# Kernel tuning notes

Measured on AMD Instinct MI355X. Metric: run time of the kernel, lower is better.

The kernel has to match this reference:

```python
import jax, jax.numpy as jnp
import numpy as np

N_NODES = 100000


def spmm(edge_src, edge_dst, edge_w, h):
    # out[d] = sum_{e: dst[e]=d} w[e] * h[src[e]]  -- sparse adj @ h
    return jax.ops.segment_sum(h[edge_src] * edge_w[:, None], edge_dst,
                               num_segments=N_NODES)


def gcn_layer(x, W, edge_src, edge_dst, edge_w, use_activation):
    support = x @ W                      # dense projection [N, out]
    out = spmm(edge_src, edge_dst, edge_w, support)
    return jax.nn.relu(out) if use_activation else out


def setup_inputs() -> dict:
    key = jax.random.key(0)
    ks = jax.random.split(key, 9)
    n_edges = 3200000

    def xavier(k, shape):
        fan_in, fan_out = shape
        a = jnp.sqrt(6.0 / (fan_in + fan_out))
        return jax.random.uniform(k, shape, jnp.float32, -a, a)

    return {
        "x": jax.random.normal(ks[0], (N_NODES, 512), jnp.float32),
        "edge_src": jax.random.randint(ks[1], (n_edges,), 0, N_NODES, jnp.int32),
        "edge_dst": jax.random.randint(ks[2], (n_edges,), 0, N_NODES, jnp.int32),
        "edge_w": jax.random.uniform(ks[3], (n_edges,), jnp.float32),
        "W1": xavier(ks[4], (512, 128)),
        "W2": xavier(ks[5], (128, 64)),
        "W3": xavier(ks[6], (64, 32)),
        "Wmu": xavier(ks[7], (32, 16)),
        "Wlv": xavier(ks[8], (32, 16)),
    }


def reference(x, edge_src, edge_dst, edge_w, W1, W2, W3, Wmu, Wlv):
    # Eval-mode GCNVAE forward: dropout is identity, z = mu.
    h1 = gcn_layer(x, W1, edge_src, edge_dst, edge_w, True)
    h2 = gcn_layer(h1, W2, edge_src, edge_dst, edge_w, True)
    h3 = gcn_layer(h2, W3, edge_src, edge_dst, edge_w, True)
    mu = gcn_layer(h3, Wmu, edge_src, edge_dst, edge_w, False)
    logvar = gcn_layer(h3, Wlv, edge_src, edge_dst, edge_w, False)
    z = mu  # reparameterize in eval mode returns mu
    return (z, mu, logvar)
```

## Files before the change

### kernel.cpp

```cpp
#include <hip/hip_runtime.h>

typedef __attribute__((ext_vector_type(4))) float floatx4;
typedef __attribute__((ext_vector_type(8))) short bf16x8;

#define NPB 256
#define CHUNK 6144
#define MAXB 12288

__device__ __forceinline__ float bf2f(unsigned short h) {
  union { unsigned int u; float f; } c; c.u = ((unsigned int)h) << 16; return c.f;
}
__device__ __forceinline__ unsigned short f2bf(float f) {
  union { float f; unsigned int u; } c; c.f = f;
  unsigned int r = c.u + 0x7FFFu + ((c.u >> 16) & 1u);
  return (unsigned short)(r >> 16);
}

__device__ __forceinline__ void gl16(const void* g, void* l) {
  __builtin_amdgcn_global_load_lds(
      (const __attribute__((address_space(1))) unsigned int*)g,
      (__attribute__((address_space(3))) unsigned int*)l, 16, 0, 0);
}


__global__ __launch_bounds__(256) void bhist_k(const int* __restrict__ dst,
                                               int* __restrict__ bcnt, int E, int B) {
  __shared__ int h[512];
  int tid = threadIdx.x;
  for (int i = tid; i < 512; i += 256) h[i] = 0;
  __syncthreads();
  for (int i = blockIdx.x * 256 + tid; i < E; i += gridDim.x * 256)
    atomicAdd(&h[dst[i] >> 8], 1);
  __syncthreads();
  for (int i = tid; i < B; i += 256)
    if (h[i]) atomicAdd(&bcnt[i], h[i]);
}

__global__ __launch_bounds__(512) void bscan_k(const int* __restrict__ bcnt,
                                               int* __restrict__ bstart,
                                               int* __restrict__ bcur, int B) {
  __shared__ int s[512];
  int tid = threadIdx.x;
  int v = (tid < B) ? bcnt[tid] : 0;
  s[tid] = v;
  __syncthreads();
  for (int off = 1; off < 512; off <<= 1) {
    int t = (tid >= off) ? s[tid - off] : 0;
    __syncthreads();
    s[tid] += t;
    __syncthreads();
  }
  int excl = s[tid] - v;
  if (tid < B) { bstart[tid] = excl; bcur[tid] = excl; }
  if (tid == 511) bstart[B] = s[511];
}

__global__ __launch_bounds__(256) void part_k(const int* __restrict__ src,
                                              const int* __restrict__ dst,
                                              const float* __restrict__ w,
                                              int* __restrict__ bcur,
                                              int2* __restrict__ prec, int E, int B) {
  __shared__ int hist[512];
  __shared__ int lstart[512];
  __shared__ int cur[512];
  __shared__ int gbase[512];
  __shared__ int ss[256];
  __shared__ int2 srt[CHUNK];
  int tid = threadIdx.x;
  int e0 = blockIdx.x * CHUNK;
  int cnt = min(CHUNK, E - e0);
  for (int i = tid; i < 512; i += 256) hist[i] = 0;
  __syncthreads();
  for (int i = tid; i < cnt; i += 256) atomicAdd(&hist[dst[e0 + i] >> 8], 1);
  __syncthreads();
  int a0 = hist[2 * tid], a1 = hist[2 * tid + 1];
  ss[tid] = a0 + a1;
  __syncthreads();
  for (int off = 1; off < 256; off <<= 1) {
    int t = (tid >= off) ? ss[tid - off] : 0;
    __syncthreads();
    ss[tid] += t;
    __syncthreads();
  }
  int excl = tid ? ss[tid - 1] : 0;
  lstart[2 * tid] = excl;     cur[2 * tid] = excl;
  lstart[2 * tid + 1] = excl + a0; cur[2 * tid + 1] = excl + a0;
  __syncthreads();
  for (int i = tid; i < B; i += 256)
    gbase[i] = hist[i] ? atomicAdd(&bcur[i], hist[i]) : 0;
  __syncthreads();
  for (int i = tid; i < cnt; i += 256) {
    int d = dst[e0 + i];
    int b = d >> 8;
    float wf = w[e0 + i];
    int w15 = (int)(wf * 32768.f + 0.5f);
    if (w15 > 32767) w15 = 32767;
    int2 r;
    r.x = src[e0 + i] | (w15 << 17);
    r.y = (b << 8) | (d & 255);
    int pos = atomicAdd(&cur[b], 1);
    srt[pos] = r;
  }
  __syncthreads();
  for (int j = tid; j < cnt; j += 256) {
    int2 r = srt[j];
    int b = r.y >> 8;
    prec[gbase[b] + (j - lstart[b])] = make_int2(r.x, r.y & 255);
  }
}

__global__ __launch_bounds__(256) void sort_k(const int2* __restrict__ prec,
                                              const int* __restrict__ bstart,
                                              unsigned int* __restrict__ recs,
                                              int* __restrict__ row_start,
                                              int* __restrict__ counts, int N, int B) {
  __shared__ int hist[256], lstart[256], cur[256], ss[256];
  __shared__ unsigned int srt[MAXB];
  int b = blockIdx.x;
  int tid = threadIdx.x;
  int s = bstart[b];
  int cnt = bstart[b + 1] - s;
  if (cnt > MAXB) cnt = MAXB;
  hist[tid] = 0;
  __syncthreads();
  for (int i = tid; i < cnt; i += 256) atomicAdd(&hist[prec[s + i].y], 1);
  __syncthreads();
  ss[tid] = hist[tid];
  __syncthreads();
  for (int off = 1; off < 256; off <<= 1) {
    int t = (tid >= off) ? ss[tid - off] : 0;
    __syncthreads();
    ss[tid] += t;
    __syncthreads();
  }
  int excl = ss[tid] - hist[tid];
  lstart[tid] = excl;
  cur[tid] = excl;
  int node = b * NPB + tid;
  if (node < N) { row_start[node] = s + excl; counts[node] = hist[tid]; }
  __syncthreads();
  for (int i = tid; i < cnt; i += 256) {
    int2 r = prec[s + i];
    int pos = atomicAdd(&cur[r.y], 1);
    srt[pos] = (unsigned int)r.x;
  }
  __syncthreads();
  for (int i = tid; i < cnt; i += 256) recs[s + i] = srt[i];
}


__global__ __launch_bounds__(256) void tw1_k(const float* __restrict__ W1,
                                             unsigned short* __restrict__ W1t) {
  int i = blockIdx.x * 256 + threadIdx.x;
  if (i >= 512 * 128) return;
  int k = i >> 7, n = i & 127;
  W1t[n * 512 + k] = f2bf(W1[i]);
}


__device__ __forceinline__ bf16x8 cvt8(float4 lo, float4 hi) {
  bf16x8 r;
  r[0] = (short)f2bf(lo.x); r[1] = (short)f2bf(lo.y);
  r[2] = (short)f2bf(lo.z); r[3] = (short)f2bf(lo.w);
  r[4] = (short)f2bf(hi.x); r[5] = (short)f2bf(hi.y);
  r[6] = (short)f2bf(hi.z); r[7] = (short)f2bf(hi.w);
  return r;
}

__global__ __launch_bounds__(256, 3) void gemm1_mfma(const float* __restrict__ A,
                                                     const unsigned short* __restrict__ W1t,
                                                     unsigned short* __restrict__ C, int N) {
  constexpr int BK = 32;
  __shared__ __align__(16) float          As[2][128 * BK];
  __shared__ __align__(16) unsigned short Bs[2][128 * BK];
  int tid = threadIdx.x;
  int lane = tid & 63;
  int w = tid >> 6;
  int m0 = lane & 15;
  int kq = lane >> 4;
  int rowBase = blockIdx.x * 128;

  floatx4 acc[8][2];
#pragma unroll
  for (int i = 0; i < 8; ++i)
#pragma unroll
    for (int j = 0; j < 2; ++j) acc[i][j] = (floatx4)0.f;

  size_t aSrc[4]; int aDst[4];
#pragma unroll
  for (int it = 0; it < 4; ++it) {
    int c = it * 256 + w * 64 + lane;
    int r = c >> 3, ch = c & 7;
    int sc = ch ^ (r & 7);
    int gr = rowBase + r;
    if (gr > N - 1) gr = N - 1;
    aSrc[it] = (size_t)gr * 512 + sc * 4;
    aDst[it] = (it * 256 + w * 64) * 4;
  }
  size_t bSrc[2]; int bDst[2];
#pragma unroll
  for (int it = 0; it < 2; ++it) {
    int c = it * 256 + w * 64 + lane;
    int n = c >> 2, ch = c & 3;
    bSrc[it] = (size_t)n * 512 + ch * 8;
    bDst[it] = (it * 256 + w * 64) * 8;
  }

  auto stage = [&](int bi, int k0) {
#pragma unroll
    for (int it = 0; it < 4; ++it) gl16(&A[aSrc[it] + k0], &As[bi][aDst[it]]);
#pragma unroll
    for (int it = 0; it < 2; ++it) gl16(&W1t[bSrc[it] + k0], &Bs[bi][bDst[it]]);
  };

  stage(0, 0);
  int cur = 0;
  for (int t = 0; t < 16; ++t) {
    if (t < 15) {
      stage(cur ^ 1, (t + 1) * BK);
      asm volatile("s_waitcnt vmcnt(6)" ::: "memory");
    } else {
      asm volatile("s_waitcnt vmcnt(0)" ::: "memory");
    }
    __builtin_amdgcn_s_barrier();

    bf16x8 bb0 = *reinterpret_cast<const bf16x8*>(&Bs[cur][(w * 32 + m0) * BK + kq * 8]);
    bf16x8 bb1 = *reinterpret_cast<const bf16x8*>(&Bs[cur][(w * 32 + 16 + m0) * BK + kq * 8]);
#pragma unroll
    for (int mi = 0; mi < 8; ++mi) {
      int row = mi * 16 + m0;
      int s = row & 7;
      float4 lo = *reinterpret_cast<const float4*>(&As[cur][row * BK + (((2 * kq) ^ s) << 2)]);
      float4 hi = *reinterpret_cast<const float4*>(&As[cur][row * BK + (((2 * kq + 1) ^ s) << 2)]);
      bf16x8 a = cvt8(lo, hi);
      acc[mi][0] = __builtin_amdgcn_mfma_f32_16x16x32_bf16(a, bb0, acc[mi][0], 0, 0, 0);
      acc[mi][1] = __builtin_amdgcn_mfma_f32_16x16x32_bf16(a, bb1, acc[mi][1], 0, 0, 0);
    }
    __builtin_amdgcn_s_barrier();
    cur ^= 1;
  }

#pragma unroll
  for (int mi = 0; mi < 8; ++mi) {
#pragma unroll
    for (int jn = 0; jn < 2; ++jn) {
      int gc = w * 32 + jn * 16 + m0;
#pragma unroll
      for (int p = 0; p < 4; ++p) {
        int gr = rowBase + mi * 16 + kq * 4 + p;
        if (gr < N) C[(size_t)gr * 128 + gc] = f2bf(acc[mi][jn][p]);
      }
    }
  }
}


template <int K, int O>
__global__ __launch_bounds__(256) void gemm_kernel(const unsigned short* __restrict__ A,
                                                   const float* __restrict__ W,
                                                   unsigned short* __restrict__ C, int N) {
  constexpr int BM = 64;
  constexpr int BK = 32;
  constexpr int TM = 4;
  constexpr int TN = O / 16;
  __shared__ float As[BK][BM];
  __shared__ float Ws[BK][O];
  int tid = threadIdx.x;
  int tx = tid % 16;
  int ty = tid / 16;
  int rowBase = blockIdx.x * BM;
  float acc[TM][TN];
#pragma unroll
  for (int i = 0; i < TM; ++i)
#pragma unroll
    for (int j = 0; j < TN; ++j) acc[i][j] = 0.f;

  for (int k0 = 0; k0 < K; k0 += BK) {
    {
      int r = tid >> 2;
      int kc = (tid & 3) * 8;
      int gr = rowBase + r;
      uint4 v = make_uint4(0u, 0u, 0u, 0u);
      if (gr < N) v = *reinterpret_cast<const uint4*>(&A[(size_t)gr * K + k0 + kc]);
      const unsigned short* pv = reinterpret_cast<const unsigned short*>(&v);
#pragma unroll
      for (int j = 0; j < 8; ++j) As[kc + j][r] = bf2f(pv[j]);
    }
    {
      constexpr int ELEMS = BK * O / 256;
      constexpr int NV = ELEMS / 4;
#pragma unroll
      for (int it = 0; it < NV; ++it) {
        int linear = (tid + it * 256) * 4;
        int kk = linear / O;
        int oo = linear % O;
        float4 v = *reinterpret_cast<const float4*>(&W[(size_t)(k0 + kk) * O + oo]);
        Ws[kk][oo + 0] = v.x; Ws[kk][oo + 1] = v.y;
        Ws[kk][oo + 2] = v.z; Ws[kk][oo + 3] = v.w;
      }
    }
    __syncthreads();
#pragma unroll
    for (int k = 0; k < BK; ++k) {
      float a[TM], w[TN];
#pragma unroll
      for (int i = 0; i < TM; ++i) a[i] = As[k][ty * TM + i];
#pragma unroll
      for (int j = 0; j < TN; ++j) w[j] = Ws[k][tx * TN + j];
#pragma unroll
      for (int i = 0; i < TM; ++i)
#pragma unroll
        for (int j = 0; j < TN; ++j) acc[i][j] += a[i] * w[j];
    }
    __syncthreads();
  }
#pragma unroll
  for (int i = 0; i < TM; ++i) {
    int gr = rowBase + ty * TM + i;
    if (gr >= N) continue;
#pragma unroll
    for (int j = 0; j < TN; j += 2) {
      unsigned int p = ((unsigned int)f2bf(acc[i][j + 1]) << 16) | f2bf(acc[i][j]);
      *reinterpret_cast<unsigned int*>(&C[(size_t)gr * O + tx * TN + j]) = p;
    }
  }
}


#define INV32768 3.0517578125e-05f

template <int O, bool RELU>
__global__ __launch_bounds__(256) void spmm_kernel(const unsigned int* __restrict__ recs,
                                                   const int* __restrict__ row_start,
                                                   const int* __restrict__ counts,
                                                   const unsigned short* __restrict__ sup,
                                                   unsigned short* __restrict__ hout, int N) {
  constexpr int SUBW = O / 2;
  constexpr int NPW = 256 / SUBW;
  constexpr int U = 8;
  int tid = threadIdx.x;
  int lane = tid % SUBW;
  int sub = tid / SUBW;
  int node = blockIdx.x * NPW + sub;
  if (node >= N) return;
  int start = row_start[node];
  int deg = counts[node];
  const unsigned int* supu = reinterpret_cast<const unsigned int*>(sup);
  const unsigned int* rp = recs + start;
  float a0 = 0.f, a1 = 0.f;
  int i = 0;
  for (; i + U <= deg; i += U) {
    unsigned int r[U];
#pragma unroll
    for (int j = 0; j < U; ++j) r[j] = rp[i + j];
    unsigned int v[U];
#pragma unroll
    for (int j = 0; j < U; ++j) v[j] = supu[(size_t)(r[j] & 0x1FFFFu) * (O / 2) + lane];
#pragma unroll
    for (int j = 0; j < U; ++j) {
      float w = (float)(r[j] >> 17) * INV32768;
      a0 += w * bf2f((unsigned short)(v[j] & 0xFFFFu));
      a1 += w * bf2f((unsigned short)(v[j] >> 16));
    }
  }
  for (; i < deg; ++i) {
    unsigned int rec = rp[i];
    float w = (float)(rec >> 17) * INV32768;
    unsigned int v = supu[(size_t)(rec & 0x1FFFFu) * (O / 2) + lane];
    a0 += w * bf2f((unsigned short)(v & 0xFFFFu));
    a1 += w * bf2f((unsigned short)(v >> 16));
  }
  if (RELU) { a0 = fmaxf(a0, 0.f); a1 = fmaxf(a1, 0.f); }
  unsigned int p = ((unsigned int)f2bf(a1) << 16) | f2bf(a0);
  reinterpret_cast<unsigned int*>(hout)[(size_t)node * (O / 2) + lane] = p;
}

__global__ __launch_bounds__(256) void spmm_mulv_kernel(const unsigned int* __restrict__ recs,
                                                        const int* __restrict__ row_start,
                                                        const int* __restrict__ counts,
                                                        const unsigned short* __restrict__ sup,
                                                        float* __restrict__ out, int N) {
  constexpr int SUBW = 16;
  constexpr int NPW = 256 / SUBW;
  constexpr int U = 8;
  int tid = threadIdx.x;
  int lane = tid % SUBW;
  int sub = tid / SUBW;
  int node = blockIdx.x * NPW + sub;
  if (node >= N) return;
  int start = row_start[node];
  int deg = counts[node];
  const unsigned int* supu = reinterpret_cast<const unsigned int*>(sup);
  const unsigned int* rp = recs + start;
  float a0 = 0.f, a1 = 0.f;
  int i = 0;
  for (; i + U <= deg; i += U) {
    unsigned int r[U];
#pragma unroll
    for (int j = 0; j < U; ++j) r[j] = rp[i + j];
    unsigned int v[U];
#pragma unroll
    for (int j = 0; j < U; ++j) v[j] = supu[(size_t)(r[j] & 0x1FFFFu) * 16 + lane];
#pragma unroll
    for (int j = 0; j < U; ++j) {
      float w = (float)(r[j] >> 17) * INV32768;
      a0 += w * bf2f((unsigned short)(v[j] & 0xFFFFu));
      a1 += w * bf2f((unsigned short)(v[j] >> 16));
    }
  }
  for (; i < deg; ++i) {
    unsigned int rec = rp[i];
    float w = (float)(rec >> 17) * INV32768;
    unsigned int v = supu[(size_t)(rec & 0x1FFFFu) * 16 + lane];
    a0 += w * bf2f((unsigned short)(v & 0xFFFFu));
    a1 += w * bf2f((unsigned short)(v >> 16));
  }
  size_t nf = (size_t)N * 16;
  if (lane < 8) {
    float2 p = make_float2(a0, a1);
    *reinterpret_cast<float2*>(&out[(size_t)node * 16 + lane * 2]) = p;
    *reinterpret_cast<float2*>(&out[nf + (size_t)node * 16 + lane * 2]) = p;
  } else {
    int l = lane - 8;
    *reinterpret_cast<float2*>(&out[2 * nf + (size_t)node * 16 + l * 2]) =
        make_float2(a0, a1);
  }
}

__global__ void packw_k(const float* __restrict__ Wmu,
                        const float* __restrict__ Wlv,
                        float* __restrict__ Wcat) {
  int i = blockIdx.x * 256 + threadIdx.x;
  if (i >= 32 * 32) return;
  int k = i / 32, o = i % 32;
  Wcat[i] = (o < 16) ? Wmu[k * 16 + o] : Wlv[k * 16 + (o - 16)];
}


extern "C" void kernel_launch(void* const* d_in, const int* in_sizes, int n_in,
                              void* d_out, int out_size, void* d_ws, size_t ws_size,
                              hipStream_t stream) {
  const float* x    = (const float*)d_in[0];
  const int* esrc   = (const int*)d_in[1];
  const int* edst   = (const int*)d_in[2];
  const float* ew   = (const float*)d_in[3];
  const float* W1   = (const float*)d_in[4];
  const float* W2   = (const float*)d_in[5];
  const float* W3   = (const float*)d_in[6];
  const float* Wmu  = (const float*)d_in[7];
  const float* Wlv  = (const float*)d_in[8];
  float* out = (float*)d_out;
  int N = in_sizes[0] / 512;
  int E = in_sizes[1];
  int B = (N + NPB - 1) / NPB;

  char* p = (char*)d_ws;
  auto alloc = [&](size_t bytes) -> char* {
    char* r = p;
    p += (bytes + 255) & ~(size_t)255;
    return r;
  };
  int*  counts = (int*)alloc((size_t)N * 4);
  int*  rowst  = (int*)alloc((size_t)N * 4);
  int*  bcnt   = (int*)alloc((size_t)(B + 1) * 4);
  int*  bstart = (int*)alloc((size_t)(B + 1) * 4);
  int*  bcur   = (int*)alloc((size_t)(B + 1) * 4);
  int2* prec   = (int2*)alloc((size_t)E * 8);
  unsigned int* recs = (unsigned int*)alloc((size_t)E * 4);
  unsigned short* bufA = (unsigned short*)alloc((size_t)N * 128 * 2);
  unsigned short* bufB = (unsigned short*)alloc((size_t)N * 128 * 2);
  unsigned short* W1t  = (unsigned short*)alloc(512 * 128 * 2);
  float* Wcat = (float*)alloc(32 * 32 * 4);

  hipMemsetAsync(bcnt, 0, (size_t)(B + 1) * 4, stream);
  bhist_k<<<256, 256, 0, stream>>>(edst, bcnt, E, B);
  bscan_k<<<1, 512, 0, stream>>>(bcnt, bstart, bcur, B);
  part_k<<<(E + CHUNK - 1) / CHUNK, 256, 0, stream>>>(esrc, edst, ew, bcur, prec, E, B);
  sort_k<<<B, 256, 0, stream>>>(prec, bstart, recs, rowst, counts, N, B);

  tw1_k<<<256, 256, 0, stream>>>(W1, W1t);
  gemm1_mfma<<<(N + 127) / 128, 256, 0, stream>>>(x, W1t, bufA, N);
  spmm_kernel<128, true><<<(N + 3) / 4, 256, 0, stream>>>(recs, rowst, counts, bufA, bufB, N);

  int gemmGrid = (N + 63) / 64;

  gemm_kernel<128, 64><<<gemmGrid, 256, 0, stream>>>(bufB, W2, bufA, N);
  spmm_kernel<64, true><<<(N + 7) / 8, 256, 0, stream>>>(recs, rowst, counts, bufA, bufB, N);

  gemm_kernel<64, 32><<<gemmGrid, 256, 0, stream>>>(bufB, W3, bufA, N);
  spmm_kernel<32, true><<<(N + 15) / 16, 256, 0, stream>>>(recs, rowst, counts, bufA, bufB, N);

  packw_k<<<4, 256, 0, stream>>>(Wmu, Wlv, Wcat);
  gemm_kernel<32, 32><<<gemmGrid, 256, 0, stream>>>(bufB, Wcat, bufA, N);
  spmm_mulv_kernel<<<(N + 15) / 16, 256, 0, stream>>>(recs, rowst, counts, bufA, out, N);
}
```

Baseline: 770.2 us.

## Rework SpMM to one wavefront per node, shrink sort buckets, enlarge GEMM tiles

```diff
diff --git a/kernel.cpp b/kernel.cpp
--- a/kernel.cpp
+++ b/kernel.cpp
@@ -3,9 +3,10 @@
 typedef __attribute__((ext_vector_type(4))) float floatx4;
 typedef __attribute__((ext_vector_type(8))) short bf16x8;
 
-#define NPB 256
-#define CHUNK 6144
-#define MAXB 12288
+#define NPB 128
+#define NBINS 1024
+#define CHUNK 4096
+#define MAXB 6144
 
 __device__ __forceinline__ float bf2f(unsigned short h) {
   union { unsigned int u; float f; } c; c.u = ((unsigned int)h) << 16; return c.f;
@@ -25,26 +26,26 @@
 
 __global__ __launch_bounds__(256) void bhist_k(const int* __restrict__ dst,
                                                int* __restrict__ bcnt, int E, int B) {
-  __shared__ int h[512];
-  int tid = threadIdx.x;
-  for (int i = tid; i < 512; i += 256) h[i] = 0;
+  __shared__ int h[NBINS];
+  int tid = threadIdx.x;
+  for (int i = tid; i < NBINS; i += 256) h[i] = 0;
   __syncthreads();
   for (int i = blockIdx.x * 256 + tid; i < E; i += gridDim.x * 256)
-    atomicAdd(&h[dst[i] >> 8], 1);
+    atomicAdd(&h[dst[i] >> 7], 1);
   __syncthreads();
   for (int i = tid; i < B; i += 256)
     if (h[i]) atomicAdd(&bcnt[i], h[i]);
 }
 
-__global__ __launch_bounds__(512) void bscan_k(const int* __restrict__ bcnt,
-                                               int* __restrict__ bstart,
-                                               int* __restrict__ bcur, int B) {
-  __shared__ int s[512];
+__global__ __launch_bounds__(1024) void bscan_k(const int* __restrict__ bcnt,
+                                                int* __restrict__ bstart,
+                                                int* __restrict__ bcur, int B) {
+  __shared__ int s[NBINS];
   int tid = threadIdx.x;
   int v = (tid < B) ? bcnt[tid] : 0;
   s[tid] = v;
   __syncthreads();
-  for (int off = 1; off < 512; off <<= 1) {
+  for (int off = 1; off < NBINS; off <<= 1) {
     int t = (tid >= off) ? s[tid - off] : 0;
     __syncthreads();
     s[tid] += t;
@@ -52,7 +53,7 @@
   }
   int excl = s[tid] - v;
   if (tid < B) { bstart[tid] = excl; bcur[tid] = excl; }
-  if (tid == 511) bstart[B] = s[511];
+  if (tid == NBINS - 1) bstart[B] = s[NBINS - 1];
 }
 
 __global__ __launch_bounds__(256) void part_k(const int* __restrict__ src,
@@ -60,21 +61,22 @@
                                               const float* __restrict__ w,
                                               int* __restrict__ bcur,
                                               int2* __restrict__ prec, int E, int B) {
-  __shared__ int hist[512];
-  __shared__ int lstart[512];
-  __shared__ int cur[512];
-  __shared__ int gbase[512];
+  __shared__ int hist[NBINS];
+  __shared__ int lstart[NBINS];
+  __shared__ int cur[NBINS];
+  __shared__ int gbase[NBINS];
   __shared__ int ss[256];
   __shared__ int2 srt[CHUNK];
   int tid = threadIdx.x;
   int e0 = blockIdx.x * CHUNK;
   int cnt = min(CHUNK, E - e0);
-  for (int i = tid; i < 512; i += 256) hist[i] = 0;
-  __syncthreads();
-  for (int i = tid; i < cnt; i += 256) atomicAdd(&hist[dst[e0 + i] >> 8], 1);
-  __syncthreads();
-  int a0 = hist[2 * tid], a1 = hist[2 * tid + 1];
-  ss[tid] = a0 + a1;
+  for (int i = tid; i < NBINS; i += 256) hist[i] = 0;
+  __syncthreads();
+  for (int i = tid; i < cnt; i += 256) atomicAdd(&hist[dst[e0 + i] >> 7], 1);
+  __syncthreads();
+  int a0 = hist[4 * tid], a1 = hist[4 * tid + 1];
+  int a2 = hist[4 * tid + 2], a3 = hist[4 * tid + 3];
+  ss[tid] = a0 + a1 + a2 + a3;
   __syncthreads();
   for (int off = 1; off < 256; off <<= 1) {
     int t = (tid >= off) ? ss[tid - off] : 0;
@@ -83,29 +85,31 @@
     __syncthreads();
   }
   int excl = tid ? ss[tid - 1] : 0;
-  lstart[2 * tid] = excl;     cur[2 * tid] = excl;
-  lstart[2 * tid + 1] = excl + a0; cur[2 * tid + 1] = excl + a0;
+  lstart[4 * tid] = excl;               cur[4 * tid] = excl;
+  lstart[4 * tid + 1] = excl + a0;      cur[4 * tid + 1] = excl + a0;
+  lstart[4 * tid + 2] = excl + a0 + a1; cur[4 * tid + 2] = excl + a0 + a1;
+  lstart[4 * tid + 3] = excl + a0 + a1 + a2; cur[4 * tid + 3] = excl + a0 + a1 + a2;
   __syncthreads();
   for (int i = tid; i < B; i += 256)
     gbase[i] = hist[i] ? atomicAdd(&bcur[i], hist[i]) : 0;
   __syncthreads();
   for (int i = tid; i < cnt; i += 256) {
     int d = dst[e0 + i];
-    int b = d >> 8;
+    int b = d >> 7;
     float wf = w[e0 + i];
     int w15 = (int)(wf * 32768.f + 0.5f);
     if (w15 > 32767) w15 = 32767;
     int2 r;
     r.x = src[e0 + i] | (w15 << 17);
-    r.y = (b << 8) | (d & 255);
+    r.y = (b << 7) | (d & 127);
     int pos = atomicAdd(&cur[b], 1);
     srt[pos] = r;
   }
   __syncthreads();
   for (int j = tid; j < cnt; j += 256) {
     int2 r = srt[j];
-    int b = r.y >> 8;
-    prec[gbase[b] + (j - lstart[b])] = make_int2(r.x, r.y & 255);
+    int b = r.y >> 7;
+    prec[gbase[b] + (j - lstart[b])] = make_int2(r.x, r.y & 127);
   }
 }
 
@@ -114,30 +118,32 @@
                                               unsigned int* __restrict__ recs,
                                               int* __restrict__ row_start,
                                               int* __restrict__ counts, int N, int B) {
-  __shared__ int hist[256], lstart[256], cur[256], ss[256];
+  __shared__ int hist[NPB], lstart[NPB], cur[NPB], ss[NPB];
   __shared__ unsigned int srt[MAXB];
   int b = blockIdx.x;
   int tid = threadIdx.x;
   int s = bstart[b];
   int cnt = bstart[b + 1] - s;
   if (cnt > MAXB) cnt = MAXB;
-  hist[tid] = 0;
+  if (tid < NPB) hist[tid] = 0;
   __syncthreads();
   for (int i = tid; i < cnt; i += 256) atomicAdd(&hist[prec[s + i].y], 1);
   __syncthreads();
-  ss[tid] = hist[tid];
-  __syncthreads();
-  for (int off = 1; off < 256; off <<= 1) {
-    int t = (tid >= off) ? ss[tid - off] : 0;
-    __syncthreads();
-    ss[tid] += t;
-    __syncthreads();
-  }
-  int excl = ss[tid] - hist[tid];
-  lstart[tid] = excl;
-  cur[tid] = excl;
-  int node = b * NPB + tid;
-  if (node < N) { row_start[node] = s + excl; counts[node] = hist[tid]; }
+  if (tid < NPB) ss[tid] = hist[tid];
+  __syncthreads();
+  for (int off = 1; off < NPB; off <<= 1) {
+    int t = (tid >= off && tid < NPB) ? ss[tid - off] : 0;
+    __syncthreads();
+    if (tid < NPB) ss[tid] += t;
+    __syncthreads();
+  }
+  if (tid < NPB) {
+    int excl = ss[tid] - hist[tid];
+    lstart[tid] = excl;
+    cur[tid] = excl;
+    int node = b * NPB + tid;
+    if (node < N) { row_start[node] = s + excl; counts[node] = hist[tid]; }
+  }
   __syncthreads();
   for (int i = tid; i < cnt; i += 256) {
     int2 r = prec[s + i];
@@ -259,11 +265,12 @@
 __global__ __launch_bounds__(256) void gemm_kernel(const unsigned short* __restrict__ A,
                                                    const float* __restrict__ W,
                                                    unsigned short* __restrict__ C, int N) {
-  constexpr int BM = 64;
+  constexpr int BM = 128;
   constexpr int BK = 32;
-  constexpr int TM = 4;
+  constexpr int TM = 8;
   constexpr int TN = O / 16;
-  __shared__ float As[BK][BM];
+  constexpr int PITCH = BM + 4;
+  __shared__ float As[BK][PITCH];
   __shared__ float Ws[BK][O];
   int tid = threadIdx.x;
   int tx = tid % 16;
@@ -277,36 +284,46 @@
 
   for (int k0 = 0; k0 < K; k0 += BK) {
     {
-      int r = tid >> 2;
-      int kc = (tid & 3) * 8;
+      int r = tid >> 1;
+      int kh = (tid & 1) * 16;
       int gr = rowBase + r;
-      uint4 v = make_uint4(0u, 0u, 0u, 0u);
-      if (gr < N) v = *reinterpret_cast<const uint4*>(&A[(size_t)gr * K + k0 + kc]);
-      const unsigned short* pv = reinterpret_cast<const unsigned short*>(&v);
-#pragma unroll
-      for (int j = 0; j < 8; ++j) As[kc + j][r] = bf2f(pv[j]);
+      uint4 u0 = make_uint4(0u, 0u, 0u, 0u), u1 = u0;
+      if (gr < N) {
+        const uint4* src = reinterpret_cast<const uint4*>(&A[(size_t)gr * K + k0 + kh]);
+        u0 = src[0]; u1 = src[1];
+      }
+      const unsigned short* p0 = reinterpret_cast<const unsigned short*>(&u0);
+      const unsigned short* p1 = reinterpret_cast<const unsigned short*>(&u1);
+#pragma unroll
+      for (int j = 0; j < 8; ++j) As[kh + j][r] = bf2f(p0[j]);
+#pragma unroll
+      for (int j = 0; j < 8; ++j) As[kh + 8 + j][r] = bf2f(p1[j]);
     }
     {
-      constexpr int ELEMS = BK * O / 256;
-      constexpr int NV = ELEMS / 4;
+      constexpr int NV = BK * O / (256 * 4);
 #pragma unroll
       for (int it = 0; it < NV; ++it) {
         int linear = (tid + it * 256) * 4;
         int kk = linear / O;
         int oo = linear % O;
         float4 v = *reinterpret_cast<const float4*>(&W[(size_t)(k0 + kk) * O + oo]);
-        Ws[kk][oo + 0] = v.x; Ws[kk][oo + 1] = v.y;
-        Ws[kk][oo + 2] = v.z; Ws[kk][oo + 3] = v.w;
+        *reinterpret_cast<float4*>(&Ws[kk][oo]) = v;
       }
     }
     __syncthreads();
 #pragma unroll
     for (int k = 0; k < BK; ++k) {
-      float a[TM], w[TN];
-#pragma unroll
-      for (int i = 0; i < TM; ++i) a[i] = As[k][ty * TM + i];
-#pragma unroll
-      for (int j = 0; j < TN; ++j) w[j] = Ws[k][tx * TN + j];
+      float4 alo = *reinterpret_cast<const float4*>(&As[k][ty * 8]);
+      float4 ahi = *reinterpret_cast<const float4*>(&As[k][ty * 8 + 4]);
+      float a[TM] = {alo.x, alo.y, alo.z, alo.w, ahi.x, ahi.y, ahi.z, ahi.w};
+      float w[TN];
+      if constexpr (TN == 4) {
+        float4 w4 = *reinterpret_cast<const float4*>(&Ws[k][tx * 4]);
+        w[0] = w4.x; w[1] = w4.y; w[2] = w4.z; w[3] = w4.w;
+      } else {
+        float2 w2 = *reinterpret_cast<const float2*>(&Ws[k][tx * 2]);
+        w[0] = w2.x; w[1] = w2.y;
+      }
 #pragma unroll
       for (int i = 0; i < TM; ++i)
 #pragma unroll
@@ -330,100 +347,118 @@
 #define INV32768 3.0517578125e-05f
 
 template <int O, bool RELU>
-__global__ __launch_bounds__(256) void spmm_kernel(const unsigned int* __restrict__ recs,
-                                                   const int* __restrict__ row_start,
-                                                   const int* __restrict__ counts,
-                                                   const unsigned short* __restrict__ sup,
-                                                   unsigned short* __restrict__ hout, int N) {
-  constexpr int SUBW = O / 2;
-  constexpr int NPW = 256 / SUBW;
-  constexpr int U = 8;
-  int tid = threadIdx.x;
-  int lane = tid % SUBW;
-  int sub = tid / SUBW;
-  int node = blockIdx.x * NPW + sub;
+__global__ __launch_bounds__(256) void spmm_x4(const unsigned int* __restrict__ recs,
+                                               const int* __restrict__ row_start,
+                                               const int* __restrict__ counts,
+                                               const unsigned short* __restrict__ sup,
+                                               unsigned short* __restrict__ hout, int N) {
+  constexpr int CH = O / 8;
+  constexpr int G = 64 / CH;
+  int tid = threadIdx.x;
+  int lane = tid & 63;
+  int wv = tid >> 6;
+  int node = blockIdx.x * 4 + wv;
   if (node >= N) return;
+  int grp = lane / CH;
+  int cl = lane % CH;
   int start = row_start[node];
   int deg = counts[node];
-  const unsigned int* supu = reinterpret_cast<const unsigned int*>(sup);
+  const uint4* supv = reinterpret_cast<const uint4*>(sup);
   const unsigned int* rp = recs + start;
-  float a0 = 0.f, a1 = 0.f;
-  int i = 0;
-  for (; i + U <= deg; i += U) {
-    unsigned int r[U];
-#pragma unroll
-    for (int j = 0; j < U; ++j) r[j] = rp[i + j];
-    unsigned int v[U];
-#pragma unroll
-    for (int j = 0; j < U; ++j) v[j] = supu[(size_t)(r[j] & 0x1FFFFu) * (O / 2) + lane];
-#pragma unroll
-    for (int j = 0; j < U; ++j) {
-      float w = (float)(r[j] >> 17) * INV32768;
-      a0 += w * bf2f((unsigned short)(v[j] & 0xFFFFu));
-      a1 += w * bf2f((unsigned short)(v[j] >> 16));
-    }
-  }
-  for (; i < deg; ++i) {
-    unsigned int rec = rp[i];
-    float w = (float)(rec >> 17) * INV32768;
-    unsigned int v = supu[(size_t)(rec & 0x1FFFFu) * (O / 2) + lane];
-    a0 += w * bf2f((unsigned short)(v & 0xFFFFu));
-    a1 += w * bf2f((unsigned short)(v >> 16));
-  }
-  if (RELU) { a0 = fmaxf(a0, 0.f); a1 = fmaxf(a1, 0.f); }
-  unsigned int p = ((unsigned int)f2bf(a1) << 16) | f2bf(a0);
-  reinterpret_cast<unsigned int*>(hout)[(size_t)node * (O / 2) + lane] = p;
-}
-
-__global__ __launch_bounds__(256) void spmm_mulv_kernel(const unsigned int* __restrict__ recs,
-                                                        const int* __restrict__ row_start,
-                                                        const int* __restrict__ counts,
-                                                        const unsigned short* __restrict__ sup,
-                                                        float* __restrict__ out, int N) {
-  constexpr int SUBW = 16;
-  constexpr int NPW = 256 / SUBW;
-  constexpr int U = 8;
-  int tid = threadIdx.x;
-  int lane = tid % SUBW;
-  int sub = tid / SUBW;
-  int node = blockIdx.x * NPW + sub;
+  float a[8];
+#pragma unroll
+  for (int j = 0; j < 8; ++j) a[j] = 0.f;
+
+  for (int i = 0; i < deg; i += 2 * G) {
+    int e0 = i + grp, e1 = i + G + grp;
+    unsigned int r0 = (e0 < deg) ? rp[e0] : 0u;
+    unsigned int r1 = (e1 < deg) ? rp[e1] : 0u;
+    uint4 v0 = supv[(size_t)(r0 & 0x1FFFFu) * CH + cl];
+    uint4 v1 = supv[(size_t)(r1 & 0x1FFFFu) * CH + cl];
+    float w0 = (float)(r0 >> 17) * INV32768;
+    float w1 = (float)(r1 >> 17) * INV32768;
+    const unsigned short* q0 = reinterpret_cast<const unsigned short*>(&v0);
+    const unsigned short* q1 = reinterpret_cast<const unsigned short*>(&v1);
+#pragma unroll
+    for (int j = 0; j < 8; ++j) a[j] += w0 * bf2f(q0[j]);
+#pragma unroll
+    for (int j = 0; j < 8; ++j) a[j] += w1 * bf2f(q1[j]);
+  }
+#pragma unroll
+  for (int d = CH; d < 64; d <<= 1)
+#pragma unroll
+    for (int j = 0; j < 8; ++j) a[j] += __shfl_xor(a[j], d);
+
+  if (grp == 0) {
+    if (RELU)
+#pragma unroll
+      for (int j = 0; j < 8; ++j) a[j] = fmaxf(a[j], 0.f);
+    uint4 o;
+    o.x = ((unsigned int)f2bf(a[1]) << 16) | f2bf(a[0]);
+    o.y = ((unsigned int)f2bf(a[3]) << 16) | f2bf(a[2]);
+    o.z = ((unsigned int)f2bf(a[5]) << 16) | f2bf(a[4]);
+    o.w = ((unsigned int)f2bf(a[7]) << 16) | f2bf(a[6]);
+    reinterpret_cast<uint4*>(hout)[(size_t)node * CH + cl] = o;
+  }
+}
+
+__global__ __launch_bounds__(256) void spmm_mulv_x4(const unsigned int* __restrict__ recs,
+                                                    const int* __restrict__ row_start,
+                                                    const int* __restrict__ counts,
+                                                    const unsigned short* __restrict__ sup,
+                                                    float* __restrict__ out, int N) {
+  constexpr int CH = 4;
+  constexpr int G = 16;
+  int tid = threadIdx.x;
+  int lane = tid & 63;
+  int wv = tid >> 6;
+  int node = blockIdx.x * 4 + wv;
   if (node >= N) return;
+  int grp = lane / CH;
+  int cl = lane % CH;
   int start = row_start[node];
   int deg = counts[node];
-  const unsigned int* supu = reinterpret_cast<const unsigned int*>(sup);
+  const uint4* supv = reinterpret_cast<const uint4*>(sup);
   const unsigned int* rp = recs + start;
-  float a0 = 0.f, a1 = 0.f;
-  int i = 0;
-  for (; i + U <= deg; i += U) {
-    unsigned int r[U];
-#pragma unroll
-    for (int j = 0; j < U; ++j) r[j] = rp[i + j];
-    unsigned int v[U];
-#pragma unroll
-    for (int j = 0; j < U; ++j) v[j] = supu[(size_t)(r[j] & 0x1FFFFu) * 16 + lane];
-#pragma unroll
-    for (int j = 0; j < U; ++j) {
-      float w = (float)(r[j] >> 17) * INV32768;
-      a0 += w * bf2f((unsigned short)(v[j] & 0xFFFFu));
-      a1 += w * bf2f((unsigned short)(v[j] >> 16));
-    }
-  }
-  for (; i < deg; ++i) {
-    unsigned int rec = rp[i];
-    float w = (float)(rec >> 17) * INV32768;
-    unsigned int v = supu[(size_t)(rec & 0x1FFFFu) * 16 + lane];
-    a0 += w * bf2f((unsigned short)(v & 0xFFFFu));
-    a1 += w * bf2f((unsigned short)(v >> 16));
-  }
-  size_t nf = (size_t)N * 16;
-  if (lane < 8) {
-    float2 p = make_float2(a0, a1);
-    *reinterpret_cast<float2*>(&out[(size_t)node * 16 + lane * 2]) = p;
-    *reinterpret_cast<float2*>(&out[nf + (size_t)node * 16 + lane * 2]) = p;
-  } else {
-    int l = lane - 8;
-    *reinterpret_cast<float2*>(&out[2 * nf + (size_t)node * 16 + l * 2]) =
-        make_float2(a0, a1);
+  float a[8];
+#pragma unroll
+  for (int j = 0; j < 8; ++j) a[j] = 0.f;
+
+  for (int i = 0; i < deg; i += 2 * G) {
+    int e0 = i + grp, e1 = i + G + grp;
+    unsigned int r0 = (e0 < deg) ? rp[e0] : 0u;
+    unsigned int r1 = (e1 < deg) ? rp[e1] : 0u;
+    uint4 v0 = supv[(size_t)(r0 & 0x1FFFFu) * CH + cl];
+    uint4 v1 = supv[(size_t)(r1 & 0x1FFFFu) * CH + cl];
+    float w0 = (float)(r0 >> 17) * INV32768;
+    float w1 = (float)(r1 >> 17) * INV32768;
+    const unsigned short* q0 = reinterpret_cast<const unsigned short*>(&v0);
+    const unsigned short* q1 = reinterpret_cast<const unsigned short*>(&v1);
+#pragma unroll
+    for (int j = 0; j < 8; ++j) a[j] += w0 * bf2f(q0[j]);
+#pragma unroll
+    for (int j = 0; j < 8; ++j) a[j] += w1 * bf2f(q1[j]);
+  }
+#pragma unroll
+  for (int d = CH; d < 64; d <<= 1)
+#pragma unroll
+    for (int j = 0; j < 8; ++j) a[j] += __shfl_xor(a[j], d);
+
+  if (grp == 0) {
+    float4 lo = make_float4(a[0], a[1], a[2], a[3]);
+    float4 hi = make_float4(a[4], a[5], a[6], a[7]);
+    size_t nf = (size_t)N * 16;
+    if (cl < 2) {
+      size_t o = (size_t)node * 16 + cl * 8;
+      *reinterpret_cast<float4*>(&out[o]) = lo;
+      *reinterpret_cast<float4*>(&out[o + 4]) = hi;
+      *reinterpret_cast<float4*>(&out[nf + o]) = lo;
+      *reinterpret_cast<float4*>(&out[nf + o + 4]) = hi;
+    } else {
+      size_t o = 2 * nf + (size_t)node * 16 + (cl - 2) * 8;
+      *reinterpret_cast<float4*>(&out[o]) = lo;
+      *reinterpret_cast<float4*>(&out[o + 4]) = hi;
+    }
   }
 }
 
@@ -474,23 +509,24 @@
 
   hipMemsetAsync(bcnt, 0, (size_t)(B + 1) * 4, stream);
   bhist_k<<<256, 256, 0, stream>>>(edst, bcnt, E, B);
-  bscan_k<<<1, 512, 0, stream>>>(bcnt, bstart, bcur, B);
+  bscan_k<<<1, NBINS, 0, stream>>>(bcnt, bstart, bcur, B);
   part_k<<<(E + CHUNK - 1) / CHUNK, 256, 0, stream>>>(esrc, edst, ew, bcur, prec, E, B);
   sort_k<<<B, 256, 0, stream>>>(prec, bstart, recs, rowst, counts, N, B);
 
+  int spmmGrid = (N + 3) / 4;
+  int gemmGrid = (N + 127) / 128;
+
   tw1_k<<<256, 256, 0, stream>>>(W1, W1t);
-  gemm1_mfma<<<(N + 127) / 128, 256, 0, stream>>>(x, W1t, bufA, N);
-  spmm_kernel<128, true><<<(N + 3) / 4, 256, 0, stream>>>(recs, rowst, counts, bufA, bufB, N);
-
-  int gemmGrid = (N + 63) / 64;
+  gemm1_mfma<<<gemmGrid, 256, 0, stream>>>(x, W1t, bufA, N);
+  spmm_x4<128, true><<<spmmGrid, 256, 0, stream>>>(recs, rowst, counts, bufA, bufB, N);
 
   gemm_kernel<128, 64><<<gemmGrid, 256, 0, stream>>>(bufB, W2, bufA, N);
-  spmm_kernel<64, true><<<(N + 7) / 8, 256, 0, stream>>>(recs, rowst, counts, bufA, bufB, N);
+  spmm_x4<64, true><<<spmmGrid, 256, 0, stream>>>(recs, rowst, counts, bufA, bufB, N);
 
   gemm_kernel<64, 32><<<gemmGrid, 256, 0, stream>>>(bufB, W3, bufA, N);
-  spmm_kernel<32, true><<<(N + 15) / 16, 256, 0, stream>>>(recs, rowst, counts, bufA, bufB, N);
+  spmm_x4<32, true><<<spmmGrid, 256, 0, stream>>>(recs, rowst, counts, bufA, bufB, N);
 
   packw_k<<<4, 256, 0, stream>>>(Wmu, Wlv, Wcat);
   gemm_kernel<32, 32><<<gemmGrid, 256, 0, stream>>>(bufB, Wcat, bufA, N);
-  spmm_mulv_kernel<<<(N + 15) / 16, 256, 0, stream>>>(recs, rowst, counts, bufA, out, N);
-}
+  spmm_mulv_x4<<<spmmGrid, 256, 0, stream>>>(recs, rowst, counts, bufA, out, N);
+}
```

Result: no change. 756.9 us (-1.7%).
